# Performance work log

Hardware: AMD Instinct MI355X
Metric: run time of the kernel (lower is better)

Reference implementation:

```python
import jax, jax.numpy as jnp
import numpy as np

N_HEADS = 16

def _rope_tables(L, head_dim, dtype):
    inv_freq = 1.0 / (10000.0 ** (jnp.arange(0, head_dim, 2, dtype=jnp.float32) / head_dim))
    t = jnp.arange(L, dtype=jnp.float32)
    freqs = jnp.outer(t, inv_freq)            # [L, head_dim/2]
    emb = jnp.concatenate([freqs, freqs], -1)  # [L, head_dim]
    return jnp.cos(emb).astype(dtype), jnp.sin(emb).astype(dtype)

def _apply_rope(x, cos, sin):
    # x: [B, L, H, hd]; cos/sin: [1, L, 1, hd]
    half = x.shape[-1] // 2
    x1, x2 = x[..., :half], x[..., half:]
    x_rot = jnp.concatenate([-x2, x1], -1)
    return x * cos + x_rot * sin

def setup_inputs() -> dict:
    key = jax.random.key(0)
    ks = jax.random.split(key, 5)
    D = 1024
    s = 0.02
    return {
        "x": jax.random.normal(ks[0], (4, 2048, D), jnp.float32),
        "w_qkv": jax.random.normal(ks[1], (3 * D, D), jnp.float32) * s,
        "b_qkv": jax.random.normal(ks[2], (3 * D,), jnp.float32) * s,
        "w_out": jax.random.normal(ks[3], (D, D), jnp.float32) * s,
        "b_out": jax.random.normal(ks[4], (D,), jnp.float32) * s,
    }

def reference(x, w_qkv, b_qkv, w_out, b_out):
    B, L, D = x.shape
    H = N_HEADS
    hd = D // H
    scale = hd ** -0.5
    qkv = (x @ w_qkv.T + b_qkv).reshape(B, L, 3, H, hd)
    q, k, v = qkv[:, :, 0], qkv[:, :, 1], qkv[:, :, 2]  # [B,L,H,hd]
    cos, sin = _rope_tables(L, hd, x.dtype)
    cos = cos[None, :, None, :]
    sin = sin[None, :, None, :]
    q = _apply_rope(q, cos, sin)
    k = _apply_rope(k, cos, sin)
    # [B,H,L,L] scores, non-causal softmax
    attn = jnp.einsum('blhd,bmhd->bhlm', q, k) * scale
    attn = jax.nn.softmax(attn, axis=-1)
    out = jnp.einsum('bhlm,bmhd->blhd', attn, v).reshape(B, L, D)
    return out @ w_out.T + b_out
```

## Files before the change

kernel.cpp:

```cpp
#include <hip/hip_runtime.h>
#include <stdint.h>

typedef __attribute__((ext_vector_type(4))) float f32x4;
typedef __attribute__((ext_vector_type(8))) short bf16x8;
typedef __attribute__((ext_vector_type(4))) short s16x4;
typedef __attribute__((ext_vector_type(4))) float fp32x4;

#define QSCALE 0.18033688f

__device__ __forceinline__ short f2bf(float f) {
    union { float f; unsigned u; } v; v.f = f;
    unsigned u = v.u;
    unsigned r = u + 0x7fffu + ((u >> 16) & 1u);
    return (short)(r >> 16);
}
__device__ __forceinline__ unsigned cvtpk(float a, float b) {
    unsigned r;
    asm("v_cvt_pk_bf16_f32 %0, %1, %2" : "=v"(r) : "v"(a), "v"(b));
    return r;
}

__device__ __forceinline__ void gld_lds16(const void* g, void* l) {
    __builtin_amdgcn_global_load_lds(
        (const __attribute__((address_space(1))) unsigned int*)(uintptr_t)g,
        (__attribute__((address_space(3))) unsigned int*)(uintptr_t)l,
        16, 0, 0);
}

__global__ __launch_bounds__(256) void prep_kernel(const float* __restrict__ x,
                                                   const float* __restrict__ wq,
                                                   const float* __restrict__ wo,
                                                   short* __restrict__ xb,
                                                   short* __restrict__ wqb,
                                                   short* __restrict__ wob,
                                                   float* __restrict__ tab) {
    int bid = blockIdx.x, tid = threadIdx.x;
    if (bid < 6144) {
        const float* in; short* out; int base;
        if (bid < 4096)      { in = x;  out = xb;  base = bid; }
        else if (bid < 5632) { in = wq; out = wqb; base = bid - 4096; }
        else                 { in = wo; out = wob; base = bid - 5632; }
        int idx = (base * 256 + tid) * 8;
        fp32x4 a = *(const fp32x4*)&in[idx];
        fp32x4 b = *(const fp32x4*)&in[idx + 4];
        union { unsigned w[4]; bf16x8 v; } u;
        u.w[0] = cvtpk(a[0], a[1]); u.w[1] = cvtpk(a[2], a[3]);
        u.w[2] = cvtpk(b[0], b[1]); u.w[3] = cvtpk(b[2], b[3]);
        *(bf16x8*)&out[idx] = u.v;
    } else {
        int idx = (bid - 6144) * 256 + tid;
        int l = idx >> 5, d = idx & 31;
        float inv = expf(-(float)d / 32.f * logf(10000.f));
        float ang = (float)l * inv;
        tab[idx * 2 + 0] = cosf(ang);
        tab[idx * 2 + 1] = sinf(ang);
    }
}

template<int MODE>
__global__ __launch_bounds__(256, 2)
void gemm_bt(const short* __restrict__ A,
             const short* __restrict__ B,
             const float* __restrict__ bias,
             void* __restrict__ Cout,
             short* __restrict__ VTout,
             const float* __restrict__ tab,
             int M, int N, int K) {
    __shared__ short lds[2 * 16384];
    const int tid = threadIdx.x;
    const int lane = tid & 63, wave = tid >> 6;
    const int i15 = lane & 15, g = lane >> 4;
    const int wr = wave >> 1, wc = wave & 1;

    const int nbx = gridDim.x;
    const int nwg = nbx * gridDim.y;
    int bid = blockIdx.y * nbx + blockIdx.x;
    int sw = (bid & 7) * (nwg >> 3) + (bid >> 3);
    const int m0 = (sw / nbx) * 128;
    const int n0 = (sw % nbx) * 128;

    const int xr3 = i15 & 3, xb2 = (i15 >> 2) & 1;
    const int cLo = g ^ xr3;
    const int aoff0 = (wr * 64 + i15) * 64 + (xb2 * 4 + cLo) * 8;
    const int aoff1 = (wr * 64 + i15) * 64 + ((1 ^ xb2) * 4 + cLo) * 8;
    const int boff0 = (wc * 64 + i15) * 64 + (xb2 * 4 + cLo) * 8;
    const int boff1 = (wc * 64 + i15) * 64 + ((1 ^ xb2) * 4 + cLo) * 8;

    const int srow = tid >> 3;
    const int ss = (tid & 7) ^ (srow & 7);
    const short* a0 = A + (size_t)(m0 + srow) * K + ss * 8;
    const short* a1 = a0 + (size_t)32 * K;
    const short* a2 = a0 + (size_t)64 * K;
    const short* a3 = a0 + (size_t)96 * K;
    const short* b0 = B + (size_t)(n0 + srow) * K + ss * 8;
    const short* b1 = b0 + (size_t)32 * K;
    const short* b2 = b0 + (size_t)64 * K;
    const short* b3 = b0 + (size_t)96 * K;

#define STAGE(slot)                                                       \
    do {                                                                  \
        gld_lds16(a0, lds + (slot) * 16384 + 0 * 2048 + wave * 512);      \
        gld_lds16(a1, lds + (slot) * 16384 + 1 * 2048 + wave * 512);      \
        gld_lds16(a2, lds + (slot) * 16384 + 2 * 2048 + wave * 512);      \
        gld_lds16(a3, lds + (slot) * 16384 + 3 * 2048 + wave * 512);      \
        gld_lds16(b0, lds + (slot) * 16384 + 8192 + 0 * 2048 + wave * 512); \
        gld_lds16(b1, lds + (slot) * 16384 + 8192 + 1 * 2048 + wave * 512); \
        gld_lds16(b2, lds + (slot) * 16384 + 8192 + 2 * 2048 + wave * 512); \
        gld_lds16(b3, lds + (slot) * 16384 + 8192 + 3 * 2048 + wave * 512); \
        a0 += 64; a1 += 64; a2 += 64; a3 += 64;                           \
        b0 += 64; b1 += 64; b2 += 64; b3 += 64;                           \
    } while (0)

    STAGE(0);

    f32x4 acc[4][4] = {};
    const int NT = K >> 6;

    for (int T = 0; T < NT; ++T) {
        const int cur = T & 1;
        if (T > 0) {
            __builtin_amdgcn_s_barrier();
            __builtin_amdgcn_sched_barrier(0);
        }
        if (T + 1 < NT) {
            STAGE(cur ^ 1);
            asm volatile("s_waitcnt vmcnt(8)" ::: "memory");
        } else {
            asm volatile("s_waitcnt vmcnt(0)" ::: "memory");
        }
        __builtin_amdgcn_s_barrier();
        __builtin_amdgcn_sched_barrier(0);

        const short* As_ = lds + cur * 16384;
        const short* Bs_ = As_ + 8192;
        bf16x8 af[4][2], bfr[4][2];
#pragma unroll
        for (int m = 0; m < 4; ++m) {
            af[m][0] = *(const bf16x8*)&As_[aoff0 + m * 1024];
            af[m][1] = *(const bf16x8*)&As_[aoff1 + m * 1024];
        }
#pragma unroll
        for (int n = 0; n < 4; ++n) {
            bfr[n][0] = *(const bf16x8*)&Bs_[boff0 + n * 1024];
            bfr[n][1] = *(const bf16x8*)&Bs_[boff1 + n * 1024];
        }
        __builtin_amdgcn_s_setprio(1);
#pragma unroll
        for (int m = 0; m < 4; ++m)
#pragma unroll
            for (int n = 0; n < 4; ++n)
#pragma unroll
                for (int ks = 0; ks < 2; ++ks)
                    acc[m][n] = __builtin_amdgcn_mfma_f32_16x16x32_bf16(af[m][ks], bfr[n][ks], acc[m][n], 0, 0, 0);
        __builtin_amdgcn_s_setprio(0);
    }
#undef STAGE

    if (MODE == 0) {
#pragma unroll
        for (int m = 0; m < 4; ++m)
#pragma unroll
            for (int n = 0; n < 4; ++n) {
                int col = n0 + wc * 64 + n * 16 + i15;
                float bcol = bias[col];
#pragma unroll
                for (int j = 0; j < 4; ++j) {
                    int row = m0 + wr * 64 + m * 16 + g * 4 + j;
                    ((float*)Cout)[(size_t)row * N + col] = acc[m][n][j] + bcol;
                }
            }
    } else {
        const int sec = n0 >> 10;
        if (sec < 2) {
            const float qs = (sec == 0) ? QSCALE : 1.0f;
            short* out = (short*)Cout;
#pragma unroll
            for (int m = 0; m < 4; ++m) {
#pragma unroll
                for (int pp = 0; pp < 2; ++pp) {
                    int d = pp * 16 + i15;
                    int collo = n0 + wc * 64 + pp * 16 + i15;
                    float blo = bias[collo], bhi = bias[collo + 32];
#pragma unroll
                    for (int j = 0; j < 4; ++j) {
                        int row = m0 + wr * 64 + m * 16 + g * 4 + j;
                        int l = row & 2047;
                        float2 cs = *(const float2*)&tab[(l * 32 + d) * 2];
                        float x1 = acc[m][pp][j] + blo;
                        float x2 = acc[m][pp + 2][j] + bhi;
                        out[(size_t)row * 3072 + collo]      = f2bf((x1 * cs.x - x2 * cs.y) * qs);
                        out[(size_t)row * 3072 + collo + 32] = f2bf((x2 * cs.x + x1 * cs.y) * qs);
                    }
                }
            }
        } else {
#pragma unroll
            for (int m = 0; m < 4; ++m) {
                int rbase = m0 + wr * 64 + m * 16 + g * 4;
                int lbase = rbase & 2047, bidx = rbase >> 11;
#pragma unroll
                for (int n = 0; n < 4; ++n) {
                    int vcol = (n0 - 2048) + wc * 64 + n * 16 + i15;
                    int h = vcol >> 6, d = vcol & 63;
                    float bb = bias[n0 + wc * 64 + n * 16 + i15];
                    union { unsigned w[2]; s16x4 v; } u;
                    u.w[0] = cvtpk(acc[m][n][0] + bb, acc[m][n][1] + bb);
                    u.w[1] = cvtpk(acc[m][n][2] + bb, acc[m][n][3] + bb);
                    *(s16x4*)&VTout[((size_t)(bidx * 16 + h) * 64 + d) * 2048 + lbase] = u.v;
                }
            }
        }
    }
}

__global__ __launch_bounds__(256, 4) void attn_kernel(const short* __restrict__ qkv,
                                                      const short* __restrict__ VT,
                                                      short* __restrict__ O) {
    __shared__ short Ks[2][64 * 64];
    __shared__ short Vs[2][64 * 64];
    int orig = blockIdx.x;
    int xcd = orig & 7, idx = orig >> 3;
    int bh = xcd * 8 + (idx >> 4), qt = idx & 15;
    int b = bh >> 4, h = bh & 15;
    int tid = threadIdx.x, lane = tid & 63, wave = tid >> 6;
    int i15 = lane & 15, g = lane >> 4;
    int q0 = qt * 128;

    size_t qbase = (size_t)(b * 2048 + q0 + wave * 32);
    bf16x8 qf[2][2];
#pragma unroll
    for (int qg = 0; qg < 2; ++qg) {
        qf[qg][0] = *(const bf16x8*)&qkv[(qbase + qg * 16 + i15) * 3072 + h * 64 + 0  + g * 8];
        qf[qg][1] = *(const bf16x8*)&qkv[(qbase + qg * 16 + i15) * 3072 + h * 64 + 32 + g * 8];
    }

    bf16x8 onesf;
#pragma unroll
    for (int e = 0; e < 8; ++e) onesf[e] = (short)0x3F80;

    const int srow = tid >> 3;
    const int ss8 = (tid & 7) ^ (srow & 7);
    const int pr0 = (srow & 0x23) | ((srow & 0x10) >> 2) | ((srow & 0x0C) << 1);
    const int sr1 = srow + 32;
    const int pr1 = (sr1 & 0x23) | ((sr1 & 0x10) >> 2) | ((sr1 & 0x0C) << 1);
    const short* kb_ = qkv + (size_t)(b * 2048) * 3072 + 1024 + h * 64 + ss8 * 8;
    const short* kp0 = kb_ + (size_t)pr0 * 3072;
    const short* kp1 = kb_ + (size_t)pr1 * 3072;
    const short* vb_ = VT + (size_t)bh * 64 * 2048 + ss8 * 8;
    const short* vp0 = vb_ + (size_t)srow * 2048;
    const short* vp1 = vb_ + (size_t)sr1 * 2048;

    const int xr3 = i15 & 3, xb2 = (i15 >> 2) & 1;
    const int cLo = g ^ xr3;
    const int o0 = i15 * 64 + (xb2 * 4 + cLo) * 8;
    const int o1 = i15 * 64 + ((1 ^ xb2) * 4 + cLo) * 8;

    f32x4 acc_o[2][4] = {};
    f32x4 acc_l[2] = {};

#define STAGE(bk, bv)                                        \
    do {                                                     \
        gld_lds16(kp0, (bk) + wave * 512);                   \
        gld_lds16(kp1, (bk) + 2048 + wave * 512);            \
        gld_lds16(vp0, (bv) + wave * 512);                   \
        gld_lds16(vp1, (bv) + 2048 + wave * 512);            \
        kp0 += (size_t)64 * 3072; kp1 += (size_t)64 * 3072;  \
        vp0 += 64; vp1 += 64;                                \
    } while (0)

    STAGE(Ks[0], Vs[0]);

    for (int t = 0; t < 32; ++t) {
        const int cur = t & 1;
        if (t > 0) {
            __builtin_amdgcn_s_barrier();
            __builtin_amdgcn_sched_barrier(0);
        }
        if (t + 1 < 32) {
            STAGE(Ks[cur ^ 1], Vs[cur ^ 1]);
            asm volatile("s_waitcnt vmcnt(4)" ::: "memory");
        } else {
            asm volatile("s_waitcnt vmcnt(0)" ::: "memory");
        }
        __builtin_amdgcn_s_barrier();
        __builtin_amdgcn_sched_barrier(0);

        const short* ks = Ks[cur];
        const short* vs = Vs[cur];

        f32x4 sa[2][4] = {};
        __builtin_amdgcn_s_setprio(1);
#pragma unroll
        for (int kb = 0; kb < 2; ++kb) {
            const int ko = kb ? o1 : o0;
            bf16x8 kf[4];
#pragma unroll
            for (int jb = 0; jb < 4; ++jb) kf[jb] = *(const bf16x8*)&ks[ko + jb * 1024];
#pragma unroll
            for (int qg = 0; qg < 2; ++qg)
#pragma unroll
                for (int jb = 0; jb < 4; ++jb)
                    sa[qg][jb] = __builtin_amdgcn_mfma_f32_16x16x32_bf16(kf[jb], qf[qg][kb], sa[qg][jb], 0, 0, 0);
        }
        __builtin_amdgcn_s_setprio(0);

        bf16x8 pf[2][2];
#pragma unroll
        for (int qg = 0; qg < 2; ++qg) {
            float p[4][4];
#pragma unroll
            for (int jb = 0; jb < 4; ++jb)
#pragma unroll
                for (int r = 0; r < 4; ++r)
                    p[jb][r] = __builtin_amdgcn_exp2f(sa[qg][jb][r]);
#pragma unroll
            for (int kb = 0; kb < 2; ++kb) {
                union { unsigned w[4]; bf16x8 v; } u;
                u.w[0] = cvtpk(p[2 * kb][0],     p[2 * kb][1]);
                u.w[1] = cvtpk(p[2 * kb][2],     p[2 * kb][3]);
                u.w[2] = cvtpk(p[2 * kb + 1][0], p[2 * kb + 1][1]);
                u.w[3] = cvtpk(p[2 * kb + 1][2], p[2 * kb + 1][3]);
                pf[qg][kb] = u.v;
            }
        }

        __builtin_amdgcn_s_setprio(1);
#pragma unroll
        for (int db = 0; db < 4; ++db) {
#pragma unroll
            for (int kb = 0; kb < 2; ++kb) {
                bf16x8 vf = *(const bf16x8*)&vs[(kb ? o1 : o0) + db * 1024];
#pragma unroll
                for (int qg = 0; qg < 2; ++qg)
                    acc_o[qg][db] = __builtin_amdgcn_mfma_f32_16x16x32_bf16(pf[qg][kb], vf, acc_o[qg][db], 0, 0, 0);
            }
        }
#pragma unroll
        for (int qg = 0; qg < 2; ++qg) {
            acc_l[qg] = __builtin_amdgcn_mfma_f32_16x16x32_bf16(pf[qg][0], onesf, acc_l[qg], 0, 0, 0);
            acc_l[qg] = __builtin_amdgcn_mfma_f32_16x16x32_bf16(pf[qg][1], onesf, acc_l[qg], 0, 0, 0);
        }
        __builtin_amdgcn_s_setprio(0);
    }
#undef STAGE

#pragma unroll
    for (int qg = 0; qg < 2; ++qg) {
        float linv4[4];
#pragma unroll
        for (int r = 0; r < 4; ++r) linv4[r] = 1.f / acc_l[qg][r];
#pragma unroll
        for (int db = 0; db < 4; ++db) {
            int ocol = h * 64 + db * 16 + i15;
#pragma unroll
            for (int r = 0; r < 4; ++r) {
                size_t orow = qbase + qg * 16 + g * 4 + r;
                O[orow * 1024 + ocol] = f2bf(acc_o[qg][db][r] * linv4[r]);
            }
        }
    }
}

extern "C" void kernel_launch(void* const* d_in, const int* in_sizes, int n_in,
                              void* d_out, int out_size, void* d_ws, size_t ws_size,
                              hipStream_t stream) {
    const float* x     = (const float*)d_in[0];
    const float* w_qkv = (const float*)d_in[1];
    const float* b_qkv = (const float*)d_in[2];
    const float* w_out = (const float*)d_in[3];
    const float* b_out = (const float*)d_in[4];

    char* ws = (char*)d_ws;
    short* qkvb = (short*)(ws);
    short* xb   = (short*)(ws + 50331648);
    short* wqb  = (short*)(ws + 67108864);
    short* wob  = (short*)(ws + 73400320);
    short* VT   = (short*)(ws + 75497472);
    float* rt   = (float*)(ws + 92274688);
    short* Ob   = xb;

    prep_kernel<<<6400, 256, 0, stream>>>(x, w_qkv, w_out, xb, wqb, wob, rt);

    gemm_bt<1><<<dim3(24, 64), 256, 0, stream>>>(xb, wqb, b_qkv, qkvb, VT, rt, 8192, 3072, 1024);
    attn_kernel<<<1024, 256, 0, stream>>>(qkvb, VT, Ob);
    gemm_bt<0><<<dim3(8, 64), 256, 0, stream>>>(Ob, wob, b_out, d_out, nullptr, nullptr, 8192, 1024, 1024);
}
```

Measured before the change: 162.4 us.

## Pre-pack x into MFMA fragment layout and load A directly to registers in QKV GEMM

```diff
diff --git a/kernel.cpp b/kernel.cpp
--- a/kernel.cpp
+++ b/kernel.cpp
@@ -30,16 +30,26 @@
 __global__ __launch_bounds__(256) void prep_kernel(const float* __restrict__ x,
                                                    const float* __restrict__ wq,
                                                    const float* __restrict__ wo,
-                                                   short* __restrict__ xb,
+                                                   short* __restrict__ xp,
                                                    short* __restrict__ wqb,
                                                    short* __restrict__ wob,
                                                    float* __restrict__ tab) {
     int bid = blockIdx.x, tid = threadIdx.x;
-    if (bid < 6144) {
+    if (bid < 4096) {
+        int idx = (bid * 256 + tid) * 8;
+        fp32x4 a = *(const fp32x4*)&x[idx];
+        fp32x4 b = *(const fp32x4*)&x[idx + 4];
+        union { unsigned w[4]; bf16x8 v; } u;
+        u.w[0] = cvtpk(a[0], a[1]); u.w[1] = cvtpk(a[2], a[3]);
+        u.w[2] = cvtpk(b[0], b[1]); u.w[3] = cvtpk(b[2], b[3]);
+        int m = idx >> 10, k0 = idx & 1023;
+        int mt = m >> 4, i15 = m & 15;
+        int kt = k0 >> 5, g = (k0 >> 3) & 3;
+        *(bf16x8*)&xp[(size_t)((mt * 32 + kt) * 64 + g * 16 + i15) * 8] = u.v;
+    } else if (bid < 6144) {
         const float* in; short* out; int base;
-        if (bid < 4096)      { in = x;  out = xb;  base = bid; }
-        else if (bid < 5632) { in = wq; out = wqb; base = bid - 4096; }
-        else                 { in = wo; out = wob; base = bid - 5632; }
+        if (bid < 5632) { in = wq; out = wqb; base = bid - 4096; }
+        else            { in = wo; out = wob; base = bid - 5632; }
         int idx = (base * 256 + tid) * 8;
         fp32x4 a = *(const fp32x4*)&in[idx];
         fp32x4 b = *(const fp32x4*)&in[idx + 4];
@@ -57,15 +67,170 @@
     }
 }
 
-template<int MODE>
+__global__ __launch_bounds__(256) void gemm_qkv(const short* __restrict__ Ap,
+                                                const short* __restrict__ B,
+                                                const float* __restrict__ bias,
+                                                short* __restrict__ out,
+                                                short* __restrict__ VTout,
+                                                const float* __restrict__ tab) {
+    constexpr int K = 1024, N = 3072, NT = 16;
+    __shared__ short lds[2 * 8192];
+    const int tid = threadIdx.x;
+    const int lane = tid & 63, wave = tid >> 6;
+    const int i15 = lane & 15, g = lane >> 4;
+    const int wr = wave >> 1, wc = wave & 1;
+
+    const int nbx = gridDim.x;
+    const int nwg = nbx * gridDim.y;
+    int bid = blockIdx.y * nbx + blockIdx.x;
+    int sw = (bid & 7) * (nwg >> 3) + (bid >> 3);
+    const int m0 = (sw / nbx) * 128;
+    const int n0 = (sw % nbx) * 128;
+
+    const int xr3 = i15 & 3, xb2 = (i15 >> 2) & 1;
+    const int cLo = g ^ xr3;
+    const int boff0 = (wc * 64 + i15) * 64 + (xb2 * 4 + cLo) * 8;
+    const int boff1 = (wc * 64 + i15) * 64 + ((1 ^ xb2) * 4 + cLo) * 8;
+
+    const int srow = tid >> 3;
+    const int ss = (tid & 7) ^ (srow & 7);
+    const short* b0 = B + (size_t)(n0 + srow) * K + ss * 8;
+    const short* b1 = b0 + (size_t)32 * K;
+    const short* b2 = b0 + (size_t)64 * K;
+    const short* b3 = b0 + (size_t)96 * K;
+
+#define STAGE_B(slot)                                                 \
+    do {                                                              \
+        gld_lds16(b0, lds + (slot) * 8192 + 0 * 2048 + wave * 512);   \
+        gld_lds16(b1, lds + (slot) * 8192 + 1 * 2048 + wave * 512);   \
+        gld_lds16(b2, lds + (slot) * 8192 + 2 * 2048 + wave * 512);   \
+        gld_lds16(b3, lds + (slot) * 8192 + 3 * 2048 + wave * 512);   \
+        b0 += 64; b1 += 64; b2 += 64; b3 += 64;                       \
+    } while (0)
+
+    const short* aP = Ap + (size_t)((m0 >> 4) + wr * 4) * 16384 + lane * 8;
+
+#define LOAD_A(dst)                                                    \
+    do {                                                               \
+        dst[0][0] = *(const bf16x8*)(aP + 0 * 16384);                  \
+        dst[0][1] = *(const bf16x8*)(aP + 0 * 16384 + 512);            \
+        dst[1][0] = *(const bf16x8*)(aP + 1 * 16384);                  \
+        dst[1][1] = *(const bf16x8*)(aP + 1 * 16384 + 512);            \
+        dst[2][0] = *(const bf16x8*)(aP + 2 * 16384);                  \
+        dst[2][1] = *(const bf16x8*)(aP + 2 * 16384 + 512);            \
+        dst[3][0] = *(const bf16x8*)(aP + 3 * 16384);                  \
+        dst[3][1] = *(const bf16x8*)(aP + 3 * 16384 + 512);            \
+        aP += 1024;                                                    \
+    } while (0)
+
+#define COMPUTE(afS, slot)                                             \
+    do {                                                               \
+        const short* Bs_ = lds + (slot) * 8192;                        \
+        bf16x8 bfr[4][2];                                              \
+        _Pragma("unroll")                                              \
+        for (int n = 0; n < 4; ++n) {                                  \
+            bfr[n][0] = *(const bf16x8*)&Bs_[boff0 + n * 1024];        \
+            bfr[n][1] = *(const bf16x8*)&Bs_[boff1 + n * 1024];        \
+        }                                                              \
+        __builtin_amdgcn_s_setprio(1);                                 \
+        _Pragma("unroll")                                              \
+        for (int m = 0; m < 4; ++m)                                    \
+            _Pragma("unroll")                                          \
+            for (int n = 0; n < 4; ++n) {                              \
+                acc[m][n] = __builtin_amdgcn_mfma_f32_16x16x32_bf16(afS[m][0], bfr[n][0], acc[m][n], 0, 0, 0); \
+                acc[m][n] = __builtin_amdgcn_mfma_f32_16x16x32_bf16(afS[m][1], bfr[n][1], acc[m][n], 0, 0, 0); \
+            }                                                          \
+        __builtin_amdgcn_s_setprio(0);                                 \
+    } while (0)
+
+    bf16x8 af0[4][2], af1[4][2];
+    f32x4 acc[4][4] = {};
+
+    LOAD_A(af0);
+    STAGE_B(0);
+
+#pragma unroll
+    for (int TT = 0; TT < 8; ++TT) {
+        if (TT > 0) {
+            __builtin_amdgcn_s_barrier();
+            __builtin_amdgcn_sched_barrier(0);
+        }
+        {
+            LOAD_A(af1);
+            STAGE_B(1);
+            __builtin_amdgcn_sched_barrier(0);
+            asm volatile("s_waitcnt vmcnt(12)" ::: "memory");
+            __builtin_amdgcn_s_barrier();
+            __builtin_amdgcn_sched_barrier(0);
+            COMPUTE(af0, 0);
+        }
+        {
+            __builtin_amdgcn_s_barrier();
+            __builtin_amdgcn_sched_barrier(0);
+            if (TT < 7) {
+                LOAD_A(af0);
+                STAGE_B(0);
+                __builtin_amdgcn_sched_barrier(0);
+                asm volatile("s_waitcnt vmcnt(12)" ::: "memory");
+            } else {
+                asm volatile("s_waitcnt vmcnt(0)" ::: "memory");
+            }
+            __builtin_amdgcn_s_barrier();
+            __builtin_amdgcn_sched_barrier(0);
+            COMPUTE(af1, 1);
+        }
+    }
+#undef STAGE_B
+#undef LOAD_A
+#undef COMPUTE
+
+    const int sec = n0 >> 10;
+    if (sec < 2) {
+        const float qs = (sec == 0) ? QSCALE : 1.0f;
+#pragma unroll
+        for (int m = 0; m < 4; ++m) {
+#pragma unroll
+            for (int pp = 0; pp < 2; ++pp) {
+                int d = pp * 16 + i15;
+                int collo = n0 + wc * 64 + pp * 16 + i15;
+                float blo = bias[collo], bhi = bias[collo + 32];
+#pragma unroll
+                for (int j = 0; j < 4; ++j) {
+                    int row = m0 + wr * 64 + m * 16 + g * 4 + j;
+                    int l = row & 2047;
+                    float2 cs = *(const float2*)&tab[(l * 32 + d) * 2];
+                    float x1 = acc[m][pp][j] + blo;
+                    float x2 = acc[m][pp + 2][j] + bhi;
+                    out[(size_t)row * 3072 + collo]      = f2bf((x1 * cs.x - x2 * cs.y) * qs);
+                    out[(size_t)row * 3072 + collo + 32] = f2bf((x2 * cs.x + x1 * cs.y) * qs);
+                }
+            }
+        }
+    } else {
+#pragma unroll
+        for (int m = 0; m < 4; ++m) {
+            int rbase = m0 + wr * 64 + m * 16 + g * 4;
+            int lbase = rbase & 2047, bidx = rbase >> 11;
+#pragma unroll
+            for (int n = 0; n < 4; ++n) {
+                int vcol = (n0 - 2048) + wc * 64 + n * 16 + i15;
+                int h = vcol >> 6, d = vcol & 63;
+                float bb = bias[n0 + wc * 64 + n * 16 + i15];
+                union { unsigned w[2]; s16x4 v; } u;
+                u.w[0] = cvtpk(acc[m][n][0] + bb, acc[m][n][1] + bb);
+                u.w[1] = cvtpk(acc[m][n][2] + bb, acc[m][n][3] + bb);
+                *(s16x4*)&VTout[((size_t)(bidx * 16 + h) * 64 + d) * 2048 + lbase] = u.v;
+            }
+        }
+    }
+}
+
 __global__ __launch_bounds__(256, 2)
-void gemm_bt(const short* __restrict__ A,
-             const short* __restrict__ B,
-             const float* __restrict__ bias,
-             void* __restrict__ Cout,
-             short* __restrict__ VTout,
-             const float* __restrict__ tab,
-             int M, int N, int K) {
+void gemm_out(const short* __restrict__ A,
+              const short* __restrict__ B,
+              const float* __restrict__ bias,
+              float* __restrict__ Cout,
+              int M, int N, int K) {
     __shared__ short lds[2 * 16384];
     const int tid = threadIdx.x;
     const int lane = tid & 63, wave = tid >> 6;
@@ -156,61 +321,18 @@
     }
 #undef STAGE
 
-    if (MODE == 0) {
-#pragma unroll
-        for (int m = 0; m < 4; ++m)
-#pragma unroll
-            for (int n = 0; n < 4; ++n) {
-                int col = n0 + wc * 64 + n * 16 + i15;
-                float bcol = bias[col];
-#pragma unroll
-                for (int j = 0; j < 4; ++j) {
-                    int row = m0 + wr * 64 + m * 16 + g * 4 + j;
-                    ((float*)Cout)[(size_t)row * N + col] = acc[m][n][j] + bcol;
-                }
-            }
-    } else {
-        const int sec = n0 >> 10;
-        if (sec < 2) {
-            const float qs = (sec == 0) ? QSCALE : 1.0f;
-            short* out = (short*)Cout;
-#pragma unroll
-            for (int m = 0; m < 4; ++m) {
-#pragma unroll
-                for (int pp = 0; pp < 2; ++pp) {
-                    int d = pp * 16 + i15;
-                    int collo = n0 + wc * 64 + pp * 16 + i15;
-                    float blo = bias[collo], bhi = bias[collo + 32];
-#pragma unroll
-                    for (int j = 0; j < 4; ++j) {
-                        int row = m0 + wr * 64 + m * 16 + g * 4 + j;
-                        int l = row & 2047;
-                        float2 cs = *(const float2*)&tab[(l * 32 + d) * 2];
-                        float x1 = acc[m][pp][j] + blo;
-                        float x2 = acc[m][pp + 2][j] + bhi;
-                        out[(size_t)row * 3072 + collo]      = f2bf((x1 * cs.x - x2 * cs.y) * qs);
-                        out[(size_t)row * 3072 + collo + 32] = f2bf((x2 * cs.x + x1 * cs.y) * qs);
-                    }
-                }
-            }
-        } else {
-#pragma unroll
-            for (int m = 0; m < 4; ++m) {
-                int rbase = m0 + wr * 64 + m * 16 + g * 4;
-                int lbase = rbase & 2047, bidx = rbase >> 11;
-#pragma unroll
-                for (int n = 0; n < 4; ++n) {
-                    int vcol = (n0 - 2048) + wc * 64 + n * 16 + i15;
-                    int h = vcol >> 6, d = vcol & 63;
-                    float bb = bias[n0 + wc * 64 + n * 16 + i15];
-                    union { unsigned w[2]; s16x4 v; } u;
-                    u.w[0] = cvtpk(acc[m][n][0] + bb, acc[m][n][1] + bb);
-                    u.w[1] = cvtpk(acc[m][n][2] + bb, acc[m][n][3] + bb);
-                    *(s16x4*)&VTout[((size_t)(bidx * 16 + h) * 64 + d) * 2048 + lbase] = u.v;
-                }
-            }
-        }
-    }
+#pragma unroll
+    for (int m = 0; m < 4; ++m)
+#pragma unroll
+        for (int n = 0; n < 4; ++n) {
+            int col = n0 + wc * 64 + n * 16 + i15;
+            float bcol = bias[col];
+#pragma unroll
+            for (int j = 0; j < 4; ++j) {
+                int row = m0 + wr * 64 + m * 16 + g * 4 + j;
+                Cout[(size_t)row * N + col] = acc[m][n][j] + bcol;
+            }
+        }
 }
 
 __global__ __launch_bounds__(256, 4) void attn_kernel(const short* __restrict__ qkv,
@@ -372,16 +494,16 @@
 
     char* ws = (char*)d_ws;
     short* qkvb = (short*)(ws);
-    short* xb   = (short*)(ws + 50331648);
+    short* xp   = (short*)(ws + 50331648);
     short* wqb  = (short*)(ws + 67108864);
     short* wob  = (short*)(ws + 73400320);
     short* VT   = (short*)(ws + 75497472);
     float* rt   = (float*)(ws + 92274688);
-    short* Ob   = xb;
-
-    prep_kernel<<<6400, 256, 0, stream>>>(x, w_qkv, w_out, xb, wqb, wob, rt);
-
-    gemm_bt<1><<<dim3(24, 64), 256, 0, stream>>>(xb, wqb, b_qkv, qkvb, VT, rt, 8192, 3072, 1024);
+    short* Ob   = xp;
+
+    prep_kernel<<<6400, 256, 0, stream>>>(x, w_qkv, w_out, xp, wqb, wob, rt);
+
+    gemm_qkv<<<dim3(24, 64), 256, 0, stream>>>(xp, wqb, b_qkv, qkvb, VT, rt);
     attn_kernel<<<1024, 256, 0, stream>>>(qkvb, VT, Ob);
-    gemm_bt<0><<<dim3(8, 64), 256, 0, stream>>>(Ob, wob, b_out, d_out, nullptr, nullptr, 8192, 1024, 1024);
-}
+    gemm_out<<<dim3(8, 64), 256, 0, stream>>>(Ob, wob, b_out, (float*)d_out, 8192, 1024, 1024);
+}
```

Measured after the change: 173.3 us. +6.8%, slower.
